# Optimization experiments

Hardware: AMD Instinct MI355X
Metric: run time of the kernel (lower is better)

The kernel has to match this reference:

```python
import jax, jax.numpy as jnp
import numpy as np

NA, NB = 4096, 4096
IN, H, E = 256, 512, 131072
NEG_SLOPE = 0.2


def setup_inputs() -> dict:
    key = jax.random.key(0)
    ks = jax.random.split(key, 32)
    f32 = jnp.float32
    nrm = lambda k, s, sc=0.05: jax.random.normal(k, s, f32) * sc
    inp = {
        'x_A': jax.random.normal(ks[0], (NA, IN), f32),
        'x_B': jax.random.normal(ks[1], (NB, IN), f32),
        'edge_AB': jax.random.randint(ks[2], (2, E), 0, NA, jnp.int32),
        'edge_BA': jax.random.randint(ks[3], (2, E), 0, NB, jnp.int32),
        'W_inA': nrm(ks[4], (H, IN)), 'b_inA': jnp.zeros((H,), f32),
        'W_inB': nrm(ks[5], (H, IN)), 'b_inB': jnp.zeros((H,), f32),
        'W_in2A': nrm(ks[6], (H, IN)), 'b_in2A': jnp.zeros((H,), f32),
        'W_in2B': nrm(ks[7], (H, IN)), 'b_in2B': jnp.zeros((H,), f32),
        'Wg1': nrm(ks[8], (H, H)), 'a_src1': nrm(ks[9], (H,)),
        'a_dst1': nrm(ks[10], (H,)), 'bg1': jnp.zeros((H,), f32),
        'Wg2': nrm(ks[11], (H, H)), 'a_src2': nrm(ks[12], (H,)),
        'a_dst2': nrm(ks[13], (H,)), 'bg2': jnp.zeros((H,), f32),
        'Wqkv': nrm(ks[14], (3 * H, H)), 'bqkv': jnp.zeros((3 * H,), f32),
        'Wo': nrm(ks[15], (H, H)), 'bo': jnp.zeros((H,), f32),
    }
    return inp


def gat_conv(x, src, dst, W, a_src, a_dst, b, n):
    # PyG GATConv, heads=1: linear transform, per-edge additive attention,
    # LeakyReLU + segment softmax over incoming edges of each dst node,
    # scatter-sum of weighted source messages. Self-loops already in src/dst.
    h = x @ W.T                                # [n, H]
    e = jax.nn.leaky_relu((h @ a_src)[src] + (h @ a_dst)[dst], NEG_SLOPE)
    m = jax.ops.segment_max(e, dst, num_segments=n)
    ex = jnp.exp(e - m[dst])
    denom = jax.ops.segment_sum(ex, dst, num_segments=n)
    alpha = ex / denom[dst]                    # [E']
    out = jax.ops.segment_sum(h[src] * alpha[:, None], dst, num_segments=n)
    return out + b


def reference(x_A, x_B, edge_AB, edge_BA, W_inA, b_inA, W_inB, b_inB,
              W_in2A, b_in2A, W_in2B, b_in2B,
              Wg1, a_src1, a_dst1, bg1, Wg2, a_src2, a_dst2, bg2,
              Wqkv, bqkv, Wo, bo):
    na, nb = x_A.shape[0], x_B.shape[0]
    n = na + nb
    l = jnp.concatenate([x_A @ W_inA.T + b_inA, x_B @ W_inB.T + b_inB], 0)
    loops = jnp.arange(n, dtype=edge_AB.dtype)
    # to_homogeneous offsets: A at 0, B at na; add self-loops (PyG default)
    src = jnp.concatenate([edge_AB[0], edge_BA[0] + na, loops])
    dst = jnp.concatenate([edge_AB[1] + na, edge_BA[1], loops])
    l = gat_conv(l, src, dst, Wg1, a_src1, a_dst1, bg1, n)
    l = gat_conv(l, src, dst, Wg2, a_src2, a_dst2, bg2, n)
    # global branch: per-type linear -> dense single-head self-attention over all nodes
    g = jnp.concatenate([x_A @ W_in2A.T + b_in2A, x_B @ W_in2B.T + b_in2B], 0)
    qkv = g @ Wqkv.T + bqkv
    q, k, v = jnp.split(qkv, 3, axis=-1)       # each [n, H]
    scale = 1.0 / jnp.sqrt(jnp.asarray(q.shape[-1], q.dtype))
    attn = jax.nn.softmax((q @ k.T) * scale, axis=-1)  # [n, n]
    g = (attn @ v) @ Wo.T + bo
    z_A = jnp.concatenate([l[:na], g[:na]], axis=1)    # [na, 2H]
    z_B = jnp.concatenate([l[na:], g[na:]], axis=1)    # [nb, 2H]
    return (z_A, z_B)
```

## Files before the change

kernel.cpp:

```cpp
#include <hip/hip_runtime.h>
#include <hip/hip_bf16.h>

#define NA_ 4096
#define NB_ 4096
#define NN_ 8192
#define EE_ 131072
#define NE_ (2*EE_ + NN_)
#define HH_ 512
#define NEG_SLOPE_ 0.2f

typedef __attribute__((ext_vector_type(4))) float f32x4;
typedef __attribute__((ext_vector_type(8))) short s16x8;

__device__ inline unsigned short f2bf(float v) {
    __hip_bfloat16 h = __float2bfloat16(v);
    return __builtin_bit_cast(unsigned short, h);
}
__device__ inline float bf2f(unsigned short u) {
    return __uint_as_float(((unsigned)u) << 16);
}

__device__ inline void edge_sd(int i, const int* __restrict__ eAB,
                               const int* __restrict__ eBA, int& s, int& d) {
    if (i < EE_)            { s = eAB[i];            d = eAB[EE_ + i] + NA_; }
    else if (i < 2 * EE_)   { int j = i - EE_; s = eBA[j] + NA_; d = eBA[EE_ + j]; }
    else                    { s = i - 2 * EE_;       d = s; }
}

struct CvtJob { const float* s; unsigned short* hi; unsigned short* lo; int n4; };
struct CvtJobs { CvtJob j[10]; };

__global__ __launch_bounds__(256) void cvt_all_k(CvtJobs jobs) {
    const CvtJob jb = jobs.j[blockIdx.y];
    int i = blockIdx.x * 256 + threadIdx.x;
    if (i >= jb.n4) return;
    float4 v = ((const float4*)jb.s)[i];
    ushort4 h;
    h.x = f2bf(v.x); h.y = f2bf(v.y); h.z = f2bf(v.z); h.w = f2bf(v.w);
    ((ushort4*)jb.hi)[i] = h;
    if (jb.lo) {
        ushort4 l;
        l.x = f2bf(v.x - bf2f(h.x));
        l.y = f2bf(v.y - bf2f(h.y));
        l.z = f2bf(v.z - bf2f(h.z));
        l.w = f2bf(v.w - bf2f(h.w));
        ((ushort4*)jb.lo)[i] = l;
    }
}

template<int BM, int BN, bool BIAS, typename OutT>
__global__ __launch_bounds__(256) void mgemm_k(
    const unsigned short* __restrict__ A, const unsigned short* __restrict__ B,
    const float* __restrict__ bias, OutT* __restrict__ C,
    int K, int lda, int ldb, int ldc)
{
    constexpr int BK = 32;
    constexpr int WM = BM / 2, WN = BN / 2;
    constexpr int AM = WM / 16, AN = WN / 16;
    constexpr int AISS = BM * 4 / 256, BISS = BN * 4 / 256;
    __shared__ unsigned short sA[BM * BK];
    __shared__ unsigned short sB[BN * BK];
    const int t = threadIdx.x, lane = t & 63, w = t >> 6;
    const int wr = w >> 1, wc = w & 1;
    const int fr = lane & 15, fq = lane >> 4;
    const int bm = blockIdx.y * BM, bn = blockIdx.x * BN;

    f32x4 acc[AM][AN];
    #pragma unroll
    for (int m = 0; m < AM; m++)
        #pragma unroll
        for (int n = 0; n < AN; n++)
            #pragma unroll
            for (int r = 0; r < 4; r++) acc[m][n][r] = 0.f;

    for (int k0 = 0; k0 < K; k0 += BK) {
        __syncthreads();
        #pragma unroll
        for (int i = 0; i < AISS; i++) {
            int slot = i * 256 + t;
            __builtin_amdgcn_global_load_lds(
                (const __attribute__((address_space(1))) unsigned int*)
                    (A + (size_t)(bm + (slot >> 2)) * lda + k0 + (slot & 3) * 8),
                (__attribute__((address_space(3))) unsigned int*)
                    (sA + (i * 256 + w * 64) * 8), 16, 0, 0);
        }
        #pragma unroll
        for (int i = 0; i < BISS; i++) {
            int slot = i * 256 + t;
            __builtin_amdgcn_global_load_lds(
                (const __attribute__((address_space(1))) unsigned int*)
                    (B + (size_t)(bn + (slot >> 2)) * ldb + k0 + (slot & 3) * 8),
                (__attribute__((address_space(3))) unsigned int*)
                    (sB + (i * 256 + w * 64) * 8), 16, 0, 0);
        }
        __syncthreads();
        s16x8 a[AM], b[AN];
        #pragma unroll
        for (int m = 0; m < AM; m++)
            a[m] = *(const s16x8*)&sA[(wr * WM + m * 16 + fr) * BK + fq * 8];
        #pragma unroll
        for (int n = 0; n < AN; n++)
            b[n] = *(const s16x8*)&sB[(wc * WN + n * 16 + fr) * BK + fq * 8];
        #pragma unroll
        for (int m = 0; m < AM; m++)
            #pragma unroll
            for (int n = 0; n < AN; n++)
                acc[m][n] = __builtin_amdgcn_mfma_f32_16x16x32_bf16(a[m], b[n], acc[m][n], 0, 0, 0);
    }

    #pragma unroll
    for (int m = 0; m < AM; m++) {
        const int row = bm + wr * WM + m * 16 + fq * 4;
        #pragma unroll
        for (int n = 0; n < AN; n++) {
            const int col = bn + wc * WN + n * 16 + fr;
            const float bv = BIAS ? bias[col] : 0.f;
            #pragma unroll
            for (int r = 0; r < 4; r++) {
                float v = acc[m][n][r] + bv;
                if constexpr (sizeof(OutT) == 2)
                    C[(size_t)(row + r) * ldc + col] = (OutT)f2bf(v);
                else
                    C[(size_t)(row + r) * ldc + col] = v;
            }
        }
    }
}

__global__ __launch_bounds__(512) void mgemm_qk_k(
    const unsigned short* __restrict__ A, const unsigned short* __restrict__ B,
    unsigned short* __restrict__ C, float* __restrict__ denom)
{
    constexpr int BK = 64;
    __shared__ unsigned short smem[32768];
    unsigned short* sA = smem;
    unsigned short* sB = smem + 16384;
    unsigned short* tile = smem;
    const int t = threadIdx.x, lane = t & 63, w = t >> 6;
    const int wr = w >> 2, wc = w & 3;
    const int fr = lane & 15, fq = lane >> 4;
    const int bm = blockIdx.y * 256, bn = blockIdx.x * 256;

    f32x4 acc[8][4];
    #pragma unroll
    for (int m = 0; m < 8; m++)
        #pragma unroll
        for (int n = 0; n < 4; n++)
            #pragma unroll
            for (int r = 0; r < 4; r++) acc[m][n][r] = 0.f;

    for (int k0 = 0; k0 < 512; k0 += BK) {
        __syncthreads();
        #pragma unroll
        for (int i = 0; i < 4; i++) {
            int s = i * 512 + t;
            int row = s >> 3, cc = s & 7;
            int gc = k0 + ((cc ^ (row & 7)) << 3);
            __builtin_amdgcn_global_load_lds(
                (const __attribute__((address_space(1))) unsigned int*)
                    (A + (size_t)(bm + row) * 512 + gc),
                (__attribute__((address_space(3))) unsigned int*)
                    (sA + (i * 512 + w * 64) * 8), 16, 0, 0);
            __builtin_amdgcn_global_load_lds(
                (const __attribute__((address_space(1))) unsigned int*)
                    (B + (size_t)(bn + row) * 512 + gc),
                (__attribute__((address_space(3))) unsigned int*)
                    (sB + (i * 512 + w * 64) * 8), 16, 0, 0);
        }
        __syncthreads();
        #pragma unroll
        for (int kk = 0; kk < 2; kk++) {
            s16x8 a[8], b[4];
            #pragma unroll
            for (int m = 0; m < 8; m++) {
                int row = wr * 128 + m * 16 + fr;
                a[m] = *(const s16x8*)&sA[row * BK + (((kk * 4 + fq) ^ (row & 7)) << 3)];
            }
            #pragma unroll
            for (int n = 0; n < 4; n++) {
                int row = wc * 64 + n * 16 + fr;
                b[n] = *(const s16x8*)&sB[row * BK + (((kk * 4 + fq) ^ (row & 7)) << 3)];
            }
            #pragma unroll
            for (int m = 0; m < 8; m++)
                #pragma unroll
                for (int n = 0; n < 4; n++)
                    acc[m][n] = __builtin_amdgcn_mfma_f32_16x16x32_bf16(a[m], b[n], acc[m][n], 0, 0, 0);
        }
    }

    #pragma unroll
    for (int h = 0; h < 4; h++) {
        __syncthreads();
        #pragma unroll
        for (int mm = 0; mm < 2; mm++) {
            const int m = h * 2 + mm;
            #pragma unroll
            for (int r = 0; r < 4; r++) {
                float rsum = 0.f;
                #pragma unroll
                for (int n = 0; n < 4; n++) {
                    float p = exp2f(acc[m][n][r]);
                    rsum += p;
                    tile[(wr * 32 + mm * 16 + fq * 4 + r) * 264 + wc * 64 + n * 16 + fr]
                        = f2bf(p);
                }
                rsum += __shfl_xor(rsum, 1);
                rsum += __shfl_xor(rsum, 2);
                rsum += __shfl_xor(rsum, 4);
                rsum += __shfl_xor(rsum, 8);
                if (fr == 0)
                    atomicAdd(&denom[bm + wr * 128 + h * 32 + mm * 16 + fq * 4 + r], rsum);
            }
        }
        __syncthreads();
        #pragma unroll
        for (int j = 0; j < 4; j++) {
            int cj = j * 512 + t;
            int row_l = cj >> 5, c16 = cj & 31;
            int grow = bm + (row_l >> 5) * 128 + h * 32 + (row_l & 31);
            *(s16x8*)(C + (size_t)grow * 8192 + bn + c16 * 8)
                = *(const s16x8*)&tile[row_l * 264 + c16 * 8];
        }
    }
}

template<bool SPLIT>
__global__ __launch_bounds__(256) void mgemm_in_k(
    const unsigned short* __restrict__ xA, const unsigned short* __restrict__ xB,
    const unsigned short* __restrict__ WA, const unsigned short* __restrict__ WB,
    const float* __restrict__ biasA, const float* __restrict__ biasB,
    unsigned short* __restrict__ o1, unsigned short* __restrict__ o2)
{
    constexpr int BK = 32;
    __shared__ unsigned short sA[128 * BK];
    __shared__ unsigned short sB[128 * BK];
    const int t = threadIdx.x, lane = t & 63, w = t >> 6;
    const int wr = w >> 1, wc = w & 1;
    const int fr = lane & 15, fq = lane >> 4;
    const int bm = blockIdx.y * 128, bn = blockIdx.x * 128;
    const bool isB = bm >= NA_;
    const unsigned short* A = isB ? xB : xA;
    const unsigned short* W = isB ? WB : WA;
    const float* bias = isB ? biasB : biasA;
    const int bml = bm - (isB ? NA_ : 0);

    f32x4 acc[4][4];
    #pragma unroll
    for (int m = 0; m < 4; m++)
        #pragma unroll
        for (int n = 0; n < 4; n++)
            #pragma unroll
            for (int r = 0; r < 4; r++) acc[m][n][r] = 0.f;

    for (int k0 = 0; k0 < 256; k0 += BK) {
        __syncthreads();
        #pragma unroll
        for (int i = 0; i < 2; i++) {
            int slot = i * 256 + t;
            __builtin_amdgcn_global_load_lds(
                (const __attribute__((address_space(1))) unsigned int*)
                    (A + (size_t)(bml + (slot >> 2)) * 256 + k0 + (slot & 3) * 8),
                (__attribute__((address_space(3))) unsigned int*)
                    (sA + (i * 256 + w * 64) * 8), 16, 0, 0);
            __builtin_amdgcn_global_load_lds(
                (const __attribute__((address_space(1))) unsigned int*)
                    (W + (size_t)(bn + (slot >> 2)) * 256 + k0 + (slot & 3) * 8),
                (__attribute__((address_space(3))) unsigned int*)
                    (sB + (i * 256 + w * 64) * 8), 16, 0, 0);
        }
        __syncthreads();
        s16x8 a[4], b[4];
        #pragma unroll
        for (int m = 0; m < 4; m++)
            a[m] = *(const s16x8*)&sA[(wr * 64 + m * 16 + fr) * BK + fq * 8];
        #pragma unroll
        for (int n = 0; n < 4; n++)
            b[n] = *(const s16x8*)&sB[(wc * 64 + n * 16 + fr) * BK + fq * 8];
        #pragma unroll
        for (int m = 0; m < 4; m++)
            #pragma unroll
            for (int n = 0; n < 4; n++)
                acc[m][n] = __builtin_amdgcn_mfma_f32_16x16x32_bf16(a[m], b[n], acc[m][n], 0, 0, 0);
    }

    #pragma unroll
    for (int m = 0; m < 4; m++) {
        const int row = bm + wr * 64 + m * 16 + fq * 4;
        #pragma unroll
        for (int n = 0; n < 4; n++) {
            const int col = bn + wc * 64 + n * 16 + fr;
            const float bv = bias[col];
            #pragma unroll
            for (int r = 0; r < 4; r++) {
                float v = acc[m][n][r] + bv;
                unsigned short hi = f2bf(v);
                o1[(size_t)(row + r) * 512 + col] = hi;
                if (SPLIT)
                    o2[(size_t)(row + r) * 512 + col] = f2bf(v - bf2f(hi));
            }
        }
    }
}

__global__ __launch_bounds__(256) void mgemm3_k(
    const unsigned short* __restrict__ Ahi, const unsigned short* __restrict__ Alo,
    const unsigned short* __restrict__ Bhi,
    unsigned short* __restrict__ Cb, const float* __restrict__ a_src,
    const float* __restrict__ a_dst, float* __restrict__ as_,
    float* __restrict__ ad_, int K, int lda, int ldb)
{
    constexpr int BM = 128, BN = 128, BK = 32;
    __shared__ unsigned short sAh[BM * BK], sAl[BM * BK];
    __shared__ unsigned short sBh[BN * BK];
    const int t = threadIdx.x, lane = t & 63, w = t >> 6;
    const int wr = w >> 1, wc = w & 1;
    const int fr = lane & 15, fq = lane >> 4;
    const int bm = blockIdx.y * BM, bn = blockIdx.x * BN;

    f32x4 acc[4][4];
    #pragma unroll
    for (int m = 0; m < 4; m++)
        #pragma unroll
        for (int n = 0; n < 4; n++)
            #pragma unroll
            for (int r = 0; r < 4; r++) acc[m][n][r] = 0.f;

    for (int k0 = 0; k0 < K; k0 += BK) {
        __syncthreads();
        #pragma unroll
        for (int i = 0; i < 2; i++) {
            int slot = i * 256 + t;
            size_t ga = (size_t)(bm + (slot >> 2)) * lda + k0 + (slot & 3) * 8;
            size_t gb = (size_t)(bn + (slot >> 2)) * ldb + k0 + (slot & 3) * 8;
            unsigned loff = (unsigned)(i * 256 + w * 64) * 8;
            __builtin_amdgcn_global_load_lds(
                (const __attribute__((address_space(1))) unsigned int*)(Ahi + ga),
                (__attribute__((address_space(3))) unsigned int*)(sAh + loff), 16, 0, 0);
            __builtin_amdgcn_global_load_lds(
                (const __attribute__((address_space(1))) unsigned int*)(Alo + ga),
                (__attribute__((address_space(3))) unsigned int*)(sAl + loff), 16, 0, 0);
            __builtin_amdgcn_global_load_lds(
                (const __attribute__((address_space(1))) unsigned int*)(Bhi + gb),
                (__attribute__((address_space(3))) unsigned int*)(sBh + loff), 16, 0, 0);
        }
        __syncthreads();
        s16x8 ah[4], al[4], bh[4];
        #pragma unroll
        for (int m = 0; m < 4; m++) {
            int o = (wr * 64 + m * 16 + fr) * BK + fq * 8;
            ah[m] = *(const s16x8*)&sAh[o];
            al[m] = *(const s16x8*)&sAl[o];
        }
        #pragma unroll
        for (int n = 0; n < 4; n++)
            bh[n] = *(const s16x8*)&sBh[(wc * 64 + n * 16 + fr) * BK + fq * 8];
        #pragma unroll
        for (int m = 0; m < 4; m++)
            #pragma unroll
            for (int n = 0; n < 4; n++) {
                acc[m][n] = __builtin_amdgcn_mfma_f32_16x16x32_bf16(ah[m], bh[n], acc[m][n], 0, 0, 0);
                acc[m][n] = __builtin_amdgcn_mfma_f32_16x16x32_bf16(al[m], bh[n], acc[m][n], 0, 0, 0);
            }
    }

    float asv[4], adv[4];
    #pragma unroll
    for (int n = 0; n < 4; n++) {
        const int col = bn + wc * 64 + n * 16 + fr;
        asv[n] = a_src[col];
        adv[n] = a_dst[col];
    }

    #pragma unroll
    for (int m = 0; m < 4; m++) {
        const int row = bm + wr * 64 + m * 16 + fq * 4;
        #pragma unroll
        for (int r = 0; r < 4; r++) {
            float s1 = 0.f, s2 = 0.f;
            #pragma unroll
            for (int n = 0; n < 4; n++) {
                const int col = bn + wc * 64 + n * 16 + fr;
                float v = acc[m][n][r];
                Cb[(size_t)(row + r) * 512 + col] = f2bf(v);
                s1 = fmaf(v, asv[n], s1);
                s2 = fmaf(v, adv[n], s2);
            }
            s1 += __shfl_xor(s1, 1); s2 += __shfl_xor(s2, 1);
            s1 += __shfl_xor(s1, 2); s2 += __shfl_xor(s2, 2);
            s1 += __shfl_xor(s1, 4); s2 += __shfl_xor(s2, 4);
            s1 += __shfl_xor(s1, 8); s2 += __shfl_xor(s2, 8);
            if (fr == 0) {
                atomicAdd(&as_[row + r], s1);
                atomicAdd(&ad_[row + r], s2);
            }
        }
    }
}

__global__ __launch_bounds__(256) void mgemm_pv_k(
    const unsigned short* __restrict__ A, const unsigned short* __restrict__ B,
    unsigned short* __restrict__ C, int kseg, size_t segstride)
{
    constexpr int BK = 64;
    __shared__ unsigned short sA[128 * BK];
    __shared__ unsigned short sB[128 * BK];
    const int t = threadIdx.x, lane = t & 63, w = t >> 6;
    const int wr = w >> 1, wc = w & 1;
    const int fr = lane & 15, fq = lane >> 4;
    const int L  = blockIdx.x + (blockIdx.y << 2) + (blockIdx.z << 6);
    const int xs = L >> 7;
    const int ys = (L & 127) & 15;
    const int zs = (L & 127) >> 4;
    const int bm = ys * 128, bn = xs * 128;
    const int kofs = zs * kseg;

    f32x4 acc[4][4];
    #pragma unroll
    for (int m = 0; m < 4; m++)
        #pragma unroll
        for (int n = 0; n < 4; n++)
            #pragma unroll
            for (int r = 0; r < 4; r++) acc[m][n][r] = 0.f;

    for (int k0 = 0; k0 < kseg; k0 += BK) {
        __syncthreads();
        #pragma unroll
        for (int i = 0; i < 4; i++) {
            int s = i * 256 + t;
            int row = s >> 3, cc = s & 7;
            int gc = kofs + k0 + ((cc ^ (row & 7)) << 3);
            __builtin_amdgcn_global_load_lds(
                (const __attribute__((address_space(1))) unsigned int*)
                    (A + (size_t)(bm + row) * 8192 + gc),
                (__attribute__((address_space(3))) unsigned int*)
                    (sA + (i * 256 + w * 64) * 8), 16, 0, 0);
            __builtin_amdgcn_global_load_lds(
                (const __attribute__((address_space(1))) unsigned int*)
                    (B + (size_t)(bn + row) * 8192 + gc),
                (__attribute__((address_space(3))) unsigned int*)
                    (sB + (i * 256 + w * 64) * 8), 16, 0, 0);
        }
        __syncthreads();
        #pragma unroll
        for (int kk = 0; kk < 2; kk++) {
            s16x8 a[4], b[4];
            #pragma unroll
            for (int m = 0; m < 4; m++) {
                int row = wr * 64 + m * 16 + fr;
                a[m] = *(const s16x8*)&sA[row * BK + (((kk * 4 + fq) ^ (row & 7)) << 3)];
            }
            #pragma unroll
            for (int n = 0; n < 4; n++) {
                int row = wc * 64 + n * 16 + fr;
                b[n] = *(const s16x8*)&sB[row * BK + (((kk * 4 + fq) ^ (row & 7)) << 3)];
            }
            #pragma unroll
            for (int m = 0; m < 4; m++)
                #pragma unroll
                for (int n = 0; n < 4; n++)
                    acc[m][n] = __builtin_amdgcn_mfma_f32_16x16x32_bf16(a[m], b[n], acc[m][n], 0, 0, 0);
        }
    }

    unsigned short* Cz = C + (size_t)zs * segstride;
    #pragma unroll
    for (int m = 0; m < 4; m++) {
        const int row = bm + wr * 64 + m * 16 + fq * 4;
        #pragma unroll
        for (int n = 0; n < 4; n++) {
            const int col = bn + wc * 64 + n * 16 + fr;
            #pragma unroll
            for (int r = 0; r < 4; r++)
                Cz[(size_t)(row + r) * 512 + col] = f2bf(acc[m][n][r]);
        }
    }
}

__global__ __launch_bounds__(256) void radd_k(const unsigned short* __restrict__ src,
                                              unsigned short* __restrict__ dst,
                                              const float* __restrict__ dn,
                                              int n8, int segs, size_t stride8) {
    int i = blockIdx.x * 256 + threadIdx.x;
    if (i >= n8) return;
    float acc[8] = {0,0,0,0,0,0,0,0};
    for (int s = 0; s < segs; s++) {
        s16x8 v = ((const s16x8*)src)[i + s * stride8];
        #pragma unroll
        for (int j = 0; j < 8; j++) acc[j] += bf2f((unsigned short)v[j]);
    }
    const float rd = 1.0f / dn[i >> 6];
    s16x8 o;
    #pragma unroll
    for (int j = 0; j < 8; j++) o[j] = (short)f2bf(acc[j] * rd);
    ((s16x8*)dst)[i] = o;
}

__global__ __launch_bounds__(256) void mgemm_qkv_k(
    const unsigned short* __restrict__ A, const unsigned short* __restrict__ B,
    const float* __restrict__ bias, float scale,
    unsigned short* __restrict__ qb, unsigned short* __restrict__ kb,
    unsigned short* __restrict__ vb)
{
    constexpr int BM = 128, BN = 128, BK = 32;
    __shared__ unsigned short sA[BM * BK];
    __shared__ unsigned short sB[BN * BK];
    const int t = threadIdx.x, lane = t & 63, w = t >> 6;
    const int wr = w >> 1, wc = w & 1;
    const int fr = lane & 15, fq = lane >> 4;
    const int bm = blockIdx.y * BM, bn = blockIdx.x * BN;

    f32x4 acc[4][4];
    #pragma unroll
    for (int m = 0; m < 4; m++)
        #pragma unroll
        for (int n = 0; n < 4; n++)
            #pragma unroll
            for (int r = 0; r < 4; r++) acc[m][n][r] = 0.f;

    for (int k0 = 0; k0 < 512; k0 += BK) {
        __syncthreads();
        #pragma unroll
        for (int i = 0; i < 2; i++) {
            int slot = i * 256 + t;
            __builtin_amdgcn_global_load_lds(
                (const __attribute__((address_space(1))) unsigned int*)
                    (A + (size_t)(bm + (slot >> 2)) * 512 + k0 + (slot & 3) * 8),
                (__attribute__((address_space(3))) unsigned int*)
                    (sA + (i * 256 + w * 64) * 8), 16, 0, 0);
            __builtin_amdgcn_global_load_lds(
                (const __attribute__((address_space(1))) unsigned int*)
                    (B + (size_t)(bn + (slot >> 2)) * 512 + k0 + (slot & 3) * 8),
                (__attribute__((address_space(3))) unsigned int*)
                    (sB + (i * 256 + w * 64) * 8), 16, 0, 0);
        }
        __syncthreads();
        s16x8 a[4], b[4];
        #pragma unroll
        for (int m = 0; m < 4; m++)
            a[m] = *(const s16x8*)&sA[(wr * 64 + m * 16 + fr) * BK + fq * 8];
        #pragma unroll
        for (int n = 0; n < 4; n++)
            b[n] = *(const s16x8*)&sB[(wc * 64 + n * 16 + fr) * BK + fq * 8];
        #pragma unroll
        for (int m = 0; m < 4; m++)
            #pragma unroll
            for (int n = 0; n < 4; n++)
                acc[m][n] = __builtin_amdgcn_mfma_f32_16x16x32_bf16(a[m], b[n], acc[m][n], 0, 0, 0);
    }

    #pragma unroll
    for (int m = 0; m < 4; m++) {
        const int row = bm + wr * 64 + m * 16 + fq * 4;
        #pragma unroll
        for (int n = 0; n < 4; n++) {
            const int col = bn + wc * 64 + n * 16 + fr;
            const float bv = bias[col];
            #pragma unroll
            for (int r = 0; r < 4; r++) {
                float v = acc[m][n][r] + bv;
                if (col < 512)
                    qb[(size_t)(row + r) * 512 + col] = f2bf(v * scale);
                else if (col < 1024)
                    kb[(size_t)(row + r) * 512 + (col - 512)] = f2bf(v);
                else
                    vb[(size_t)(row + r) * 512 + (col - 1024)] = f2bf(v);
            }
        }
    }
}

__global__ __launch_bounds__(256) void trT_k(const unsigned short* __restrict__ vb,
                                             unsigned short* __restrict__ vT) {
    __shared__ unsigned short s[64][65];
    const int t = threadIdx.x;
    const int rowo = blockIdx.y * 64;
    const int colo = blockIdx.x * 64;
    {
        int r = t >> 2, cg = (t & 3) * 16;
        const s16x8* src = (const s16x8*)(vb + (size_t)(rowo + r) * 512 + colo + cg);
        s16x8 u0 = src[0], u1 = src[1];
        #pragma unroll
        for (int j = 0; j < 8; j++) {
            s[r][cg + j]     = (unsigned short)u0[j];
            s[r][cg + 8 + j] = (unsigned short)u1[j];
        }
    }
    __syncthreads();
    {
        int c = t >> 2, rg = (t & 3) * 16;
        s16x8 o0, o1;
        #pragma unroll
        for (int j = 0; j < 8; j++) {
            o0[j] = (short)s[rg + j][c];
            o1[j] = (short)s[rg + 8 + j][c];
        }
        s16x8* dst = (s16x8*)(vT + (size_t)(colo + c) * 8192 + rowo + rg);
        dst[0] = o0; dst[1] = o1;
    }
}

__global__ void count_deg_k(const int* eAB, const int* eBA, int* deg) {
    int i = blockIdx.x * 256 + threadIdx.x;
    if (i >= NE_) return;
    int s, d; edge_sd(i, eAB, eBA, s, d);
    atomicAdd(&deg[d], 1);
}

__global__ __launch_bounds__(256) void scan_k(const int* __restrict__ deg, int* rowstart) {
    __shared__ int part[256];
    int t = threadIdx.x;
    int base = t * 32;
    int loc[32]; int s = 0;
    #pragma unroll
    for (int j = 0; j < 32; j++) { loc[j] = s; s += deg[base + j]; }
    part[t] = s;
    __syncthreads();
    if (t == 0) {
        int a = 0;
        for (int i = 0; i < 256; i++) { int v = part[i]; part[i] = a; a += v; }
        rowstart[NN_] = a;
    }
    __syncthreads();
    int off = part[t];
    #pragma unroll
    for (int j = 0; j < 32; j++) rowstart[base + j] = off + loc[j];
}

__global__ void fill_csr_k(const int* eAB, const int* eBA,
                           const int* __restrict__ rowstart, int* cursor,
                           int* csr_src, int* pos) {
    int i = blockIdx.x * 256 + threadIdx.x;
    if (i >= NE_) return;
    int s, d; edge_sd(i, eAB, eBA, s, d);
    int p = atomicAdd(&cursor[d], 1);
    int slot = rowstart[d] + p;
    csr_src[slot] = s;
    pos[i] = slot;
}

__global__ void edge_fused_k(const int* eAB, const int* eBA,
                             const float* __restrict__ as_, const float* __restrict__ ad_,
                             const int* __restrict__ pos,
                             float* __restrict__ evs, float* __restrict__ denom) {
    int i = blockIdx.x * 256 + threadIdx.x;
    if (i >= NE_) return;
    int s, d; edge_sd(i, eAB, eBA, s, d);
    float e = as_[s] + ad_[d];
    e = (e >= 0.f) ? e : NEG_SLOPE_ * e;
    float ex = expf(e);
    evs[pos[i]] = ex;
    atomicAdd(&denom[d], ex);
}

template<bool SPLIT>
__global__ __launch_bounds__(256) void gat_agg_k(
    const int* __restrict__ rowstart, const int* __restrict__ csr_src,
    const float* __restrict__ evs, const float* __restrict__ denom,
    const unsigned short* __restrict__ hb, const float* __restrict__ bias,
    float* __restrict__ outF, int ldo,
    unsigned short* __restrict__ outHi, unsigned short* __restrict__ outLo)
{
    int wid  = (blockIdx.x * 256 + threadIdx.x) >> 6;
    int lane = threadIdx.x & 63;
    if (wid >= NN_) return;
    float acc[8] = {0.f,0.f,0.f,0.f,0.f,0.f,0.f,0.f};
    int beg = rowstart[wid], end = rowstart[wid + 1];
    float rden = 1.0f / denom[wid];
    int p = beg;
    for (; p + 1 < end; p += 2) {
        int s0 = csr_src[p], s1 = csr_src[p + 1];
        float al0 = evs[p] * rden, al1 = evs[p + 1] * rden;
        s16x8 h0 = *(const s16x8*)(hb + (size_t)s0 * HH_ + lane * 8);
        s16x8 h1 = *(const s16x8*)(hb + (size_t)s1 * HH_ + lane * 8);
        #pragma unroll
        for (int j = 0; j < 8; j++)
            acc[j] = fmaf(al1, bf2f((unsigned short)h1[j]),
                     fmaf(al0, bf2f((unsigned short)h0[j]), acc[j]));
    }
    if (p < end) {
        int s0 = csr_src[p];
        float al0 = evs[p] * rden;
        s16x8 h0 = *(const s16x8*)(hb + (size_t)s0 * HH_ + lane * 8);
        #pragma unroll
        for (int j = 0; j < 8; j++)
            acc[j] = fmaf(al0, bf2f((unsigned short)h0[j]), acc[j]);
    }
    #pragma unroll
    for (int j = 0; j < 8; j++) acc[j] += bias[lane * 8 + j];
    if (SPLIT) {
        s16x8 hi, lo;
        #pragma unroll
        for (int j = 0; j < 8; j++) {
            unsigned short h = f2bf(acc[j]);
            hi[j] = (short)h;
            lo[j] = (short)f2bf(acc[j] - bf2f(h));
        }
        *(s16x8*)(outHi + (size_t)wid * HH_ + lane * 8) = hi;
        *(s16x8*)(outLo + (size_t)wid * HH_ + lane * 8) = lo;
    } else {
        float* o = outF + (size_t)wid * ldo + lane * 8;
        *(float4*)(o)     = make_float4(acc[0], acc[1], acc[2], acc[3]);
        *(float4*)(o + 4) = make_float4(acc[4], acc[5], acc[6], acc[7]);
    }
}

extern "C" void kernel_launch(void* const* d_in, const int* in_sizes, int n_in,
                              void* d_out, int out_size, void* d_ws, size_t ws_size,
                              hipStream_t stream)
{
    const float* x_A    = (const float*)d_in[0];
    const float* x_B    = (const float*)d_in[1];
    const int*   eAB    = (const int*)d_in[2];
    const int*   eBA    = (const int*)d_in[3];
    const float* W_inA  = (const float*)d_in[4];  const float* b_inA  = (const float*)d_in[5];
    const float* W_inB  = (const float*)d_in[6];  const float* b_inB  = (const float*)d_in[7];
    const float* W_in2A = (const float*)d_in[8];  const float* b_in2A = (const float*)d_in[9];
    const float* W_in2B = (const float*)d_in[10]; const float* b_in2B = (const float*)d_in[11];
    const float* Wg1    = (const float*)d_in[12]; const float* a_src1 = (const float*)d_in[13];
    const float* a_dst1 = (const float*)d_in[14]; const float* bg1    = (const float*)d_in[15];
    const float* Wg2    = (const float*)d_in[16]; const float* a_src2 = (const float*)d_in[17];
    const float* a_dst2 = (const float*)d_in[18]; const float* bg2    = (const float*)d_in[19];
    const float* Wqkv   = (const float*)d_in[20]; const float* bqkv   = (const float*)d_in[21];
    const float* Wo     = (const float*)d_in[22]; const float* bo     = (const float*)d_in[23];

    float* out = (float*)d_out;

    char* base = (char*)d_ws;
    size_t off = 0;
    auto alloc = [&](size_t nb) -> char* {
        char* p = base + off;
        off = (off + nb + 255) & ~(size_t)255;
        return p;
    };

    float*          bufA  = (float*)alloc((size_t)NN_ * 512 * 4);
    float*          bufB  = (float*)alloc((size_t)NN_ * 512 * 4);
    float*          bufC  = (float*)alloc((size_t)NN_ * 512 * 4);
    float*          as_   = (float*)alloc(NN_ * 4);
    float*          ad_   = (float*)alloc(NN_ * 4);
    float*          denom = (float*)alloc(NN_ * 4);
    int*            deg   = (int*)alloc(NN_ * 4);
    int*            cursor= (int*)alloc(NN_ * 4);
    float*          cdn   = (float*)alloc(NN_ * 4);
    int*            rowst = (int*)alloc((NN_ + 1) * 4);
    int*            csrs  = (int*)alloc((size_t)NE_ * 4);
    int*            pos   = (int*)alloc((size_t)NE_ * 4);
    float*          evs   = (float*)alloc((size_t)NE_ * 4);
    unsigned short* xbA   = (unsigned short*)alloc((size_t)NA_ * 256 * 2);
    unsigned short* xbB   = (unsigned short*)alloc((size_t)NB_ * 256 * 2);
    unsigned short* WbinA = (unsigned short*)alloc((size_t)512 * 256 * 2);
    unsigned short* WbinB = (unsigned short*)alloc((size_t)512 * 256 * 2);
    unsigned short* Wbin2A= (unsigned short*)alloc((size_t)512 * 256 * 2);
    unsigned short* Wbin2B= (unsigned short*)alloc((size_t)512 * 256 * 2);
    unsigned short* Wbqkv = (unsigned short*)alloc((size_t)1536 * 512 * 2);
    unsigned short* Wbo   = (unsigned short*)alloc((size_t)512 * 512 * 2);
    unsigned short* Wg1b  = (unsigned short*)alloc((size_t)512 * 512 * 2);
    unsigned short* Wg2b  = (unsigned short*)alloc((size_t)512 * 512 * 2);
    unsigned short* qb    = (unsigned short*)alloc((size_t)NN_ * 512 * 2);
    unsigned short* kb    = (unsigned short*)alloc((size_t)NN_ * 512 * 2);
    unsigned short* vT    = (unsigned short*)alloc((size_t)512 * NN_ * 2);
    unsigned short* ab    = (unsigned short*)alloc((size_t)NN_ * 512 * 2);

    unsigned short* hb = vT;
    unsigned short* gb = (unsigned short*)bufC;
    unsigned short* vb = gb + (size_t)NN_ * 512;
    unsigned short* Sb = (unsigned short*)bufA;
    unsigned short* pv = (unsigned short*)bufC;

    const int R = 2048, SEGS = 8, KSEG = 8192 / SEGS;
    const int EG = (NE_ + 255) / 256;
    const float scale2 = 0.044194173824159216f * 1.4426950408889634f;

    CvtJobs jobs;
    jobs.j[0] = { x_A,    xbA,    nullptr, NA_ * 256 / 4 };
    jobs.j[1] = { x_B,    xbB,    nullptr, NB_ * 256 / 4 };
    jobs.j[2] = { W_inA,  WbinA,  nullptr, 512 * 256 / 4 };
    jobs.j[3] = { W_inB,  WbinB,  nullptr, 512 * 256 / 4 };
    jobs.j[4] = { W_in2A, Wbin2A, nullptr, 512 * 256 / 4 };
    jobs.j[5] = { W_in2B, Wbin2B, nullptr, 512 * 256 / 4 };
    jobs.j[6] = { Wqkv,   Wbqkv,  nullptr, 1536 * 512 / 4 };
    jobs.j[7] = { Wo,     Wbo,    nullptr, 512 * 512 / 4 };
    jobs.j[8] = { Wg1,    Wg1b,   nullptr, 512 * 512 / 4 };
    jobs.j[9] = { Wg2,    Wg2b,   nullptr, 512 * 512 / 4 };
    cvt_all_k<<<dim3(NA_ * 256 / 4 / 256, 10), 256, 0, stream>>>(jobs);

    hipMemsetAsync(as_, 0, (size_t)NN_ * 4 * 6, stream);

    count_deg_k<<<EG, 256, 0, stream>>>(eAB, eBA, deg);
    scan_k<<<1, 256, 0, stream>>>(deg, rowst);
    fill_csr_k<<<EG, 256, 0, stream>>>(eAB, eBA, rowst, cursor, csrs, pos);

    mgemm_in_k<true><<<dim3(4, 64), 256, 0, stream>>>(
        xbA, xbB, WbinA, WbinB, b_inA, b_inB, qb, kb);
    mgemm3_k<<<dim3(4, 64), 256, 0, stream>>>(qb, kb, Wg1b,
                                              hb, a_src1, a_dst1, as_, ad_,
                                              512, 512, 512);
    edge_fused_k<<<EG, 256, 0, stream>>>(eAB, eBA, as_, ad_, pos, evs, denom);
    gat_agg_k<true><<<NN_/4, 256, 0, stream>>>(rowst, csrs, evs, denom,
                                               hb, bg1, nullptr, 0, qb, kb);
    hipMemsetAsync(as_, 0, NN_ * 12, stream);
    mgemm3_k<<<dim3(4, 64), 256, 0, stream>>>(qb, kb, Wg2b,
                                              hb, a_src2, a_dst2, as_, ad_,
                                              512, 512, 512);
    edge_fused_k<<<EG, 256, 0, stream>>>(eAB, eBA, as_, ad_, pos, evs, denom);
    gat_agg_k<false><<<NN_/4, 256, 0, stream>>>(rowst, csrs, evs, denom,
                                                hb, bg2, out, 1024, nullptr, nullptr);

    mgemm_in_k<false><<<dim3(4, 64), 256, 0, stream>>>(
        xbA, xbB, Wbin2A, Wbin2B, b_in2A, b_in2B, gb, nullptr);
    mgemm_qkv_k<<<dim3(12, 64), 256, 0, stream>>>(gb, Wbqkv, bqkv, scale2, qb, kb, vb);
    trT_k<<<dim3(8, 128), 256, 0, stream>>>(vb, vT);
    for (int c0 = 0; c0 < 8192; c0 += R) {
        float* dn = cdn + c0;
        mgemm_qk_k<<<dim3(32, 8), 512, 0, stream>>>(
            qb + (size_t)c0 * 512, kb, Sb, dn);
        mgemm_pv_k<<<dim3(4, R/128, SEGS), 256, 0, stream>>>(
            Sb, vT, pv, KSEG, (size_t)R * 512);
        radd_k<<<(R*512/8 + 255)/256, 256, 0, stream>>>(
            pv, ab + (size_t)c0 * 512, dn, R*512/8, SEGS, (size_t)R*512/8);
    }
    mgemm_k<128,128,true,float><<<dim3(4, 64), 256, 0, stream>>>(
        ab, Wbo, bo, out + 512, 512, 512, 512, 1024);
}
```

Baseline: 563.2 us.

## Double-buffer LDS staging in the QK, split-precision GAT and PV GEMM kernels

Converts three MFMA GEMM kernels (the fused QK^T/exp kernel, the hi/lo split-precision GAT linear, and the split-K attention-times-V kernel) from single-buffered load-then-compute loops to double-buffered pipelines. The next K-slice is loaded into the other LDS buffer while MFMAs run on the current one, with one barrier per step instead of two. BK drops to 32 with a 4-way XOR swizzle, and s_setprio raises wave priority around the MFMA block. This is meant to hide global-to-LDS latency, at the cost of twice as many loop iterations and a sync on every step. A GLOAD16 macro is added to tidy up the other load sites.

```diff
diff --git a/kernel.cpp b/kernel.cpp
--- a/kernel.cpp
+++ b/kernel.cpp
@@ -19,6 +19,11 @@
 __device__ inline float bf2f(unsigned short u) {
     return __uint_as_float(((unsigned)u) << 16);
 }
+
+#define GLOAD16(gsrc, ldst)                                                    \
+    __builtin_amdgcn_global_load_lds(                                          \
+        (const __attribute__((address_space(1))) unsigned int*)(gsrc),         \
+        (__attribute__((address_space(3))) unsigned int*)(ldst), 16, 0, 0)
 
 __device__ inline void edge_sd(int i, const int* __restrict__ eAB,
                                const int* __restrict__ eBA, int& s, int& d) {
@@ -78,20 +83,14 @@
         #pragma unroll
         for (int i = 0; i < AISS; i++) {
             int slot = i * 256 + t;
-            __builtin_amdgcn_global_load_lds(
-                (const __attribute__((address_space(1))) unsigned int*)
-                    (A + (size_t)(bm + (slot >> 2)) * lda + k0 + (slot & 3) * 8),
-                (__attribute__((address_space(3))) unsigned int*)
-                    (sA + (i * 256 + w * 64) * 8), 16, 0, 0);
+            GLOAD16(A + (size_t)(bm + (slot >> 2)) * lda + k0 + (slot & 3) * 8,
+                    sA + (i * 256 + w * 64) * 8);
         }
         #pragma unroll
         for (int i = 0; i < BISS; i++) {
             int slot = i * 256 + t;
-            __builtin_amdgcn_global_load_lds(
-                (const __attribute__((address_space(1))) unsigned int*)
-                    (B + (size_t)(bn + (slot >> 2)) * ldb + k0 + (slot & 3) * 8),
-                (__attribute__((address_space(3))) unsigned int*)
-                    (sB + (i * 256 + w * 64) * 8), 16, 0, 0);
+            GLOAD16(B + (size_t)(bn + (slot >> 2)) * ldb + k0 + (slot & 3) * 8,
+                    sB + (i * 256 + w * 64) * 8);
         }
         __syncthreads();
         s16x8 a[AM], b[AN];
@@ -131,10 +130,8 @@
     const unsigned short* __restrict__ A, const unsigned short* __restrict__ B,
     unsigned short* __restrict__ C, float* __restrict__ denom)
 {
-    constexpr int BK = 64;
+    constexpr int BK = 32;
     __shared__ unsigned short smem[32768];
-    unsigned short* sA = smem;
-    unsigned short* sB = smem + 16384;
     unsigned short* tile = smem;
     const int t = threadIdx.x, lane = t & 63, w = t >> 6;
     const int wr = w >> 2, wc = w & 3;
@@ -149,44 +146,48 @@
             #pragma unroll
             for (int r = 0; r < 4; r++) acc[m][n][r] = 0.f;
 
+    auto stage = [&](int buf, int k0) {
+        unsigned short* dA = smem + buf * 16384;
+        unsigned short* dB = dA + 8192;
+        #pragma unroll
+        for (int i = 0; i < 2; i++) {
+            int s = i * 512 + t;
+            int row = s >> 2, cc = s & 3;
+            int gc = k0 + ((cc ^ (row & 3)) << 3);
+            GLOAD16(A + (size_t)(bm + row) * 512 + gc, dA + (i * 512 + w * 64) * 8);
+            GLOAD16(B + (size_t)(bn + row) * 512 + gc, dB + (i * 512 + w * 64) * 8);
+        }
+    };
+
+    stage(0, 0);
+    asm volatile("s_waitcnt vmcnt(0)" ::: "memory");
+    __builtin_amdgcn_s_barrier();
+    int cur = 0;
     for (int k0 = 0; k0 < 512; k0 += BK) {
-        __syncthreads();
-        #pragma unroll
-        for (int i = 0; i < 4; i++) {
-            int s = i * 512 + t;
-            int row = s >> 3, cc = s & 7;
-            int gc = k0 + ((cc ^ (row & 7)) << 3);
-            __builtin_amdgcn_global_load_lds(
-                (const __attribute__((address_space(1))) unsigned int*)
-                    (A + (size_t)(bm + row) * 512 + gc),
-                (__attribute__((address_space(3))) unsigned int*)
-                    (sA + (i * 512 + w * 64) * 8), 16, 0, 0);
-            __builtin_amdgcn_global_load_lds(
-                (const __attribute__((address_space(1))) unsigned int*)
-                    (B + (size_t)(bn + row) * 512 + gc),
-                (__attribute__((address_space(3))) unsigned int*)
-                    (sB + (i * 512 + w * 64) * 8), 16, 0, 0);
-        }
-        __syncthreads();
-        #pragma unroll
-        for (int kk = 0; kk < 2; kk++) {
-            s16x8 a[8], b[4];
-            #pragma unroll
-            for (int m = 0; m < 8; m++) {
-                int row = wr * 128 + m * 16 + fr;
-                a[m] = *(const s16x8*)&sA[row * BK + (((kk * 4 + fq) ^ (row & 7)) << 3)];
-            }
-            #pragma unroll
-            for (int n = 0; n < 4; n++) {
-                int row = wc * 64 + n * 16 + fr;
-                b[n] = *(const s16x8*)&sB[row * BK + (((kk * 4 + fq) ^ (row & 7)) << 3)];
-            }
-            #pragma unroll
-            for (int m = 0; m < 8; m++)
-                #pragma unroll
-                for (int n = 0; n < 4; n++)
-                    acc[m][n] = __builtin_amdgcn_mfma_f32_16x16x32_bf16(a[m], b[n], acc[m][n], 0, 0, 0);
-        }
+        if (k0 + BK < 512) stage(cur ^ 1, k0 + BK);
+        const unsigned short* rA = smem + cur * 16384;
+        const unsigned short* rB = rA + 8192;
+        s16x8 a[8], b[4];
+        #pragma unroll
+        for (int m = 0; m < 8; m++) {
+            int row = wr * 128 + m * 16 + fr;
+            a[m] = *(const s16x8*)&rA[row * BK + ((fq ^ (row & 3)) << 3)];
+        }
+        #pragma unroll
+        for (int n = 0; n < 4; n++) {
+            int row = wc * 64 + n * 16 + fr;
+            b[n] = *(const s16x8*)&rB[row * BK + ((fq ^ (row & 3)) << 3)];
+        }
+        __builtin_amdgcn_s_setprio(1);
+        #pragma unroll
+        for (int m = 0; m < 8; m++)
+            #pragma unroll
+            for (int n = 0; n < 4; n++)
+                acc[m][n] = __builtin_amdgcn_mfma_f32_16x16x32_bf16(a[m], b[n], acc[m][n], 0, 0, 0);
+        __builtin_amdgcn_s_setprio(0);
+        asm volatile("s_waitcnt vmcnt(0)" ::: "memory");
+        __builtin_amdgcn_s_barrier();
+        cur ^= 1;
     }
 
     #pragma unroll
@@ -258,16 +259,10 @@
         #pragma unroll
         for (int i = 0; i < 2; i++) {
             int slot = i * 256 + t;
-            __builtin_amdgcn_global_load_lds(
-                (const __attribute__((address_space(1))) unsigned int*)
-                    (A + (size_t)(bml + (slot >> 2)) * 256 + k0 + (slot & 3) * 8),
-                (__attribute__((address_space(3))) unsigned int*)
-                    (sA + (i * 256 + w * 64) * 8), 16, 0, 0);
-            __builtin_amdgcn_global_load_lds(
-                (const __attribute__((address_space(1))) unsigned int*)
-                    (W + (size_t)(bn + (slot >> 2)) * 256 + k0 + (slot & 3) * 8),
-                (__attribute__((address_space(3))) unsigned int*)
-                    (sB + (i * 256 + w * 64) * 8), 16, 0, 0);
+            GLOAD16(A + (size_t)(bml + (slot >> 2)) * 256 + k0 + (slot & 3) * 8,
+                    sA + (i * 256 + w * 64) * 8);
+            GLOAD16(W + (size_t)(bn + (slot >> 2)) * 256 + k0 + (slot & 3) * 8,
+                    sB + (i * 256 + w * 64) * 8);
         }
         __syncthreads();
         s16x8 a[4], b[4];
@@ -310,13 +305,12 @@
     const float* __restrict__ a_dst, float* __restrict__ as_,
     float* __restrict__ ad_, int K, int lda, int ldb)
 {
-    constexpr int BM = 128, BN = 128, BK = 32;
-    __shared__ unsigned short sAh[BM * BK], sAl[BM * BK];
-    __shared__ unsigned short sBh[BN * BK];
+    constexpr int BK = 32;
+    __shared__ unsigned short smem[24576];
     const int t = threadIdx.x, lane = t & 63, w = t >> 6;
     const int wr = w >> 1, wc = w & 1;
     const int fr = lane & 15, fq = lane >> 4;
-    const int bm = blockIdx.y * BM, bn = blockIdx.x * BN;
+    const int bm = blockIdx.y * 128, bn = blockIdx.x * 128;
 
     f32x4 acc[4][4];
     #pragma unroll
@@ -326,35 +320,47 @@
             #pragma unroll
             for (int r = 0; r < 4; r++) acc[m][n][r] = 0.f;
 
+    auto stage = [&](int buf, int k0) {
+        unsigned short* dAh = smem + buf * 12288;
+        unsigned short* dAl = dAh + 4096;
+        unsigned short* dBh = dAh + 8192;
+        #pragma unroll
+        for (int i = 0; i < 2; i++) {
+            int s = i * 256 + t;
+            int row = s >> 2, cc = s & 3;
+            int gco = (cc ^ (row & 3)) << 3;
+            size_t ga = (size_t)(bm + row) * lda + k0 + gco;
+            size_t gb = (size_t)(bn + row) * ldb + k0 + gco;
+            unsigned loff = (unsigned)(i * 256 + w * 64) * 8;
+            GLOAD16(Ahi + ga, dAh + loff);
+            GLOAD16(Alo + ga, dAl + loff);
+            GLOAD16(Bhi + gb, dBh + loff);
+        }
+    };
+
+    stage(0, 0);
+    asm volatile("s_waitcnt vmcnt(0)" ::: "memory");
+    __builtin_amdgcn_s_barrier();
+    int cur = 0;
     for (int k0 = 0; k0 < K; k0 += BK) {
-        __syncthreads();
-        #pragma unroll
-        for (int i = 0; i < 2; i++) {
-            int slot = i * 256 + t;
-            size_t ga = (size_t)(bm + (slot >> 2)) * lda + k0 + (slot & 3) * 8;
-            size_t gb = (size_t)(bn + (slot >> 2)) * ldb + k0 + (slot & 3) * 8;
-            unsigned loff = (unsigned)(i * 256 + w * 64) * 8;
-            __builtin_amdgcn_global_load_lds(
-                (const __attribute__((address_space(1))) unsigned int*)(Ahi + ga),
-                (__attribute__((address_space(3))) unsigned int*)(sAh + loff), 16, 0, 0);
-            __builtin_amdgcn_global_load_lds(
-                (const __attribute__((address_space(1))) unsigned int*)(Alo + ga),
-                (__attribute__((address_space(3))) unsigned int*)(sAl + loff), 16, 0, 0);
-            __builtin_amdgcn_global_load_lds(
-                (const __attribute__((address_space(1))) unsigned int*)(Bhi + gb),
-                (__attribute__((address_space(3))) unsigned int*)(sBh + loff), 16, 0, 0);
-        }
-        __syncthreads();
+        if (k0 + BK < K) stage(cur ^ 1, k0 + BK);
+        const unsigned short* rAh = smem + cur * 12288;
+        const unsigned short* rAl = rAh + 4096;
+        const unsigned short* rBh = rAh + 8192;
         s16x8 ah[4], al[4], bh[4];
         #pragma unroll
         for (int m = 0; m < 4; m++) {
-            int o = (wr * 64 + m * 16 + fr) * BK + fq * 8;
-            ah[m] = *(const s16x8*)&sAh[o];
-            al[m] = *(const s16x8*)&sAl[o];
-        }
-        #pragma unroll
-        for (int n = 0; n < 4; n++)
-            bh[n] = *(const s16x8*)&sBh[(wc * 64 + n * 16 + fr) * BK + fq * 8];
+            int row = wr * 64 + m * 16 + fr;
+            int o = row * BK + ((fq ^ (row & 3)) << 3);
+            ah[m] = *(const s16x8*)&rAh[o];
+            al[m] = *(const s16x8*)&rAl[o];
+        }
+        #pragma unroll
+        for (int n = 0; n < 4; n++) {
+            int row = wc * 64 + n * 16 + fr;
+            bh[n] = *(const s16x8*)&rBh[row * BK + ((fq ^ (row & 3)) << 3)];
+        }
+        __builtin_amdgcn_s_setprio(1);
         #pragma unroll
         for (int m = 0; m < 4; m++)
             #pragma unroll
@@ -362,6 +368,10 @@
                 acc[m][n] = __builtin_amdgcn_mfma_f32_16x16x32_bf16(ah[m], bh[n], acc[m][n], 0, 0, 0);
                 acc[m][n] = __builtin_amdgcn_mfma_f32_16x16x32_bf16(al[m], bh[n], acc[m][n], 0, 0, 0);
             }
+        __builtin_amdgcn_s_setprio(0);
+        asm volatile("s_waitcnt vmcnt(0)" ::: "memory");
+        __builtin_amdgcn_s_barrier();
+        cur ^= 1;
     }
 
     float asv[4], adv[4];
@@ -402,9 +412,8 @@
     const unsigned short* __restrict__ A, const unsigned short* __restrict__ B,
     unsigned short* __restrict__ C, int kseg, size_t segstride)
 {
-    constexpr int BK = 64;
-    __shared__ unsigned short sA[128 * BK];
-    __shared__ unsigned short sB[128 * BK];
+    constexpr int BK = 32;
+    __shared__ unsigned short smem[16384];
     const int t = threadIdx.x, lane = t & 63, w = t >> 6;
     const int wr = w >> 1, wc = w & 1;
     const int fr = lane & 15, fq = lane >> 4;
@@ -423,44 +432,48 @@
             #pragma unroll
             for (int r = 0; r < 4; r++) acc[m][n][r] = 0.f;
 
+    auto stage = [&](int buf, int k0) {
+        unsigned short* dA = smem + buf * 8192;
+        unsigned short* dB = dA + 4096;
+        #pragma unroll
+        for (int i = 0; i < 2; i++) {
+            int s = i * 256 + t;
+            int row = s >> 2, cc = s & 3;
+            int gc = kofs + k0 + ((cc ^ (row & 3)) << 3);
+            GLOAD16(A + (size_t)(bm + row) * 8192 + gc, dA + (i * 256 + w * 64) * 8);
+            GLOAD16(B + (size_t)(bn + row) * 8192 + gc, dB + (i * 256 + w * 64) * 8);
+        }
+    };
+
+    stage(0, 0);
+    asm volatile("s_waitcnt vmcnt(0)" ::: "memory");
+    __builtin_amdgcn_s_barrier();
+    int cur = 0;
     for (int k0 = 0; k0 < kseg; k0 += BK) {
-        __syncthreads();
-        #pragma unroll
-        for (int i = 0; i < 4; i++) {
-            int s = i * 256 + t;
-            int row = s >> 3, cc = s & 7;
-            int gc = kofs + k0 + ((cc ^ (row & 7)) << 3);
-            __builtin_amdgcn_global_load_lds(
-                (const __attribute__((address_space(1))) unsigned int*)
-                    (A + (size_t)(bm + row) * 8192 + gc),
-                (__attribute__((address_space(3))) unsigned int*)
-                    (sA + (i * 256 + w * 64) * 8), 16, 0, 0);
-            __builtin_amdgcn_global_load_lds(
-                (const __attribute__((address_space(1))) unsigned int*)
-                    (B + (size_t)(bn + row) * 8192 + gc),
-                (__attribute__((address_space(3))) unsigned int*)
-                    (sB + (i * 256 + w * 64) * 8), 16, 0, 0);
-        }
-        __syncthreads();
-        #pragma unroll
-        for (int kk = 0; kk < 2; kk++) {
-            s16x8 a[4], b[4];
-            #pragma unroll
-            for (int m = 0; m < 4; m++) {
-                int row = wr * 64 + m * 16 + fr;
-                a[m] = *(const s16x8*)&sA[row * BK + (((kk * 4 + fq) ^ (row & 7)) << 3)];
-            }
-            #pragma unroll
-            for (int n = 0; n < 4; n++) {
-                int row = wc * 64 + n * 16 + fr;
-                b[n] = *(const s16x8*)&sB[row * BK + (((kk * 4 + fq) ^ (row & 7)) << 3)];
-            }
-            #pragma unroll
-            for (int m = 0; m < 4; m++)
-                #pragma unroll
-                for (int n = 0; n < 4; n++)
-                    acc[m][n] = __builtin_amdgcn_mfma_f32_16x16x32_bf16(a[m], b[n], acc[m][n], 0, 0, 0);
-        }
+        if (k0 + BK < kseg) stage(cur ^ 1, k0 + BK);
+        const unsigned short* rA = smem + cur * 8192;
+        const unsigned short* rB = rA + 4096;
+        s16x8 a[4], b[4];
+        #pragma unroll
+        for (int m = 0; m < 4; m++) {
+            int row = wr * 64 + m * 16 + fr;
+            a[m] = *(const s16x8*)&rA[row * BK + ((fq ^ (row & 3)) << 3)];
+        }
+        #pragma unroll
+        for (int n = 0; n < 4; n++) {
+            int row = wc * 64 + n * 16 + fr;
+            b[n] = *(const s16x8*)&rB[row * BK + ((fq ^ (row & 3)) << 3)];
+        }
+        __builtin_amdgcn_s_setprio(1);
+        #pragma unroll
+        for (int m = 0; m < 4; m++)
+            #pragma unroll
+            for (int n = 0; n < 4; n++)
+                acc[m][n] = __builtin_amdgcn_mfma_f32_16x16x32_bf16(a[m], b[n], acc[m][n], 0, 0, 0);
+        __builtin_amdgcn_s_setprio(0);
+        asm volatile("s_waitcnt vmcnt(0)" ::: "memory");
+        __builtin_amdgcn_s_barrier();
+        cur ^= 1;
     }
 
     unsigned short* Cz = C + (size_t)zs * segstride;
@@ -523,16 +536,10 @@
         #pragma unroll
         for (int i = 0; i < 2; i++) {
             int slot = i * 256 + t;
-            __builtin_amdgcn_global_load_lds(
-                (const __attribute__((address_space(1))) unsigned int*)
-                    (A + (size_t)(bm + (slot >> 2)) * 512 + k0 + (slot & 3) * 8),
-                (__attribute__((address_space(3))) unsigned int*)
-                    (sA + (i * 256 + w * 64) * 8), 16, 0, 0);
-            __builtin_amdgcn_global_load_lds(
-                (const __attribute__((address_space(1))) unsigned int*)
-                    (B + (size_t)(bn + (slot >> 2)) * 512 + k0 + (slot & 3) * 8),
-                (__attribute__((address_space(3))) unsigned int*)
-                    (sB + (i * 256 + w * 64) * 8), 16, 0, 0);
+            GLOAD16(A + (size_t)(bm + (slot >> 2)) * 512 + k0 + (slot & 3) * 8,
+                    sA + (i * 256 + w * 64) * 8);
+            GLOAD16(B + (size_t)(bn + (slot >> 2)) * 512 + k0 + (slot & 3) * 8,
+                    sB + (i * 256 + w * 64) * 8);
         }
         __syncthreads();
         s16x8 a[4], b[4];
```

Result: faster. 539.9 us (-4.1%).
